# Optimization experiments

Measured on AMD Instinct MI355X. Metric: run time of the kernel, lower is better.

Reference implementation:

```python
import jax, jax.numpy as jnp
import numpy as np

VOXEL_SCALE = 20.0   # cfg.SPARSE3D.VOXEL_SCALE (metric -> voxel pixels)
POOLER_SCALE = 0.25  # cfg.MODEL.ROI_BOX_HEAD.POOLER_SCALES_SPATIAL[0]
RES = 7              # pooler resolution per axis
EPS = 1e-5           # BatchNorm eps


def _roi_align_3d(feat, boxes_px, batch_idx, res):
    """3D ROIAlign, sampling_ratio=1 (one trilinear sample per bin).
    feat: [B, X, Y, Z, C] channels-last; boxes_px: [N,6] = (x1,y1,z1,x2,y2,z2)
    in feature-map coordinates. Returns [N, C, res, res, res]."""
    B, X, Y, Z, C = feat.shape
    N = boxes_px.shape[0]
    start, end = boxes_px[:, :3], boxes_px[:, 3:]
    size = jnp.maximum(end - start, 1.0)            # [N,3] legacy min roi size
    binsz = size / res
    off = jnp.arange(res, dtype=boxes_px.dtype) + 0.5
    px = start[:, 0:1] + off[None, :] * binsz[:, 0:1]   # [N,res]
    py = start[:, 1:2] + off[None, :] * binsz[:, 1:2]
    pz = start[:, 2:3] + off[None, :] * binsz[:, 2:3]
    P = res * res * res
    PX = jnp.broadcast_to(px[:, :, None, None], (N, res, res, res)).reshape(N, P)
    PY = jnp.broadcast_to(py[:, None, :, None], (N, res, res, res)).reshape(N, P)
    PZ = jnp.broadcast_to(pz[:, None, None, :], (N, res, res, res)).reshape(N, P)

    def corners(p, dim):
        p0 = jnp.floor(p)
        frac = p - p0
        i0 = jnp.clip(p0.astype(jnp.int32), 0, dim - 1)
        i1 = jnp.clip(p0.astype(jnp.int32) + 1, 0, dim - 1)
        return i0, i1, frac

    x0, x1, lx = corners(PX, X)
    y0, y1, ly = corners(PY, Y)
    z0, z1, lz = corners(PZ, Z)
    feat_flat = feat.reshape(B * X * Y * Z, C)
    base = batch_idx.astype(jnp.int32)[:, None]          # [N,1]
    acc = jnp.zeros((N, P, C), feat.dtype)
    for dx in (0, 1):  # 8 trilinear corners; fixed small loop
        xi, wx = (x0, 1.0 - lx) if dx == 0 else (x1, lx)
        for dy in (0, 1):
            yi, wy = (y0, 1.0 - ly) if dy == 0 else (y1, ly)
            for dz in (0, 1):
                zi, wz = (z0, 1.0 - lz) if dz == 0 else (z1, lz)
                lin = ((base * X + xi) * Y + yi) * Z + zi  # [N,P]
                acc = acc + (wx * wy * wz)[:, :, None] * feat_flat[lin]
    pooled = acc.reshape(N, res, res, res, C)  # 1 sample per bin -> no avg
    return pooled.transpose(0, 4, 1, 2, 3)     # [N, C, rx, ry, rz]


def setup_inputs():
    key = jax.random.key(0)
    ks = jax.random.split(key, 8)
    B, C, X, Y, Z = 2, 128, 80, 80, 20
    N, rep = 1024, 128 * RES              # rep = OUT_CHANNELS * pooler_z = 896
    in_size = C * RES * RES * RES         # 43904
    features = jax.random.normal(ks[0], (B, X, Y, Z, C), jnp.float32)
    ext = jnp.array([16.0, 16.0, 4.0], jnp.float32)  # metric extent = dim/(voxel_scale*pooler_scale)
    ctr = jax.random.uniform(ks[1], (N, 3), jnp.float32) * ext
    half = 0.25 + jax.random.uniform(ks[2], (N, 3), jnp.float32) * 1.75
    boxes = jnp.concatenate([ctr - half, ctr + half], axis=1)  # metric units
    batch_idx = jax.random.randint(ks[3], (N,), 0, B, jnp.int32)
    conv_w = jax.random.normal(ks[4], (rep, C, RES), jnp.float32) * 0.02
    conv_b = jnp.zeros((rep,), jnp.float32)
    gamma = jnp.ones((rep,), jnp.float32)
    beta = jnp.zeros((rep,), jnp.float32)
    fc6_w = jax.random.normal(ks[5], (in_size, rep), jnp.float32) * np.float32(1.0 / np.sqrt(in_size))
    fc6_b = jnp.zeros((rep,), jnp.float32)
    fc7_w = jax.random.normal(ks[6], (rep, rep), jnp.float32) * np.float32(1.0 / np.sqrt(rep))
    fc7_b = jnp.zeros((rep,), jnp.float32)
    return dict(features=features, boxes=boxes, conv_w=conv_w, conv_b=conv_b,
                gamma=gamma, beta=beta, fc6_w=fc6_w, fc6_b=fc6_b,
                fc7_w=fc7_w, fc7_b=fc7_b, batch_idx=batch_idx)


def reference(features, boxes, conv_w, conv_b, gamma, beta,
              fc6_w, fc6_b, fc7_w, fc7_b, batch_idx):
    # convert_metric_to_pixel (x voxel_scale) fused with pooler spatial scale
    boxes_px = boxes * (VOXEL_SCALE * POOLER_SCALE)
    pooled = _roi_align_3d(features, boxes_px, batch_idx, RES)  # [N,C,7,7,7]
    # conv3d kernel [1,1,Z]: contract channels and z -> [N, rep, 7, 7]
    y = jnp.einsum('ncxyz,rcz->nrxy', pooled, conv_w) + conv_b[None, :, None, None]
    # BatchNorm3d, training-mode batch statistics per channel
    mu = y.mean(axis=(0, 2, 3), keepdims=True)
    var = ((y - mu) ** 2).mean(axis=(0, 2, 3), keepdims=True)
    y = (y - mu) * jax.lax.rsqrt(var + EPS) * gamma[None, :, None, None] + beta[None, :, None, None]
    y = jax.nn.relu(y)
    x2 = y.reshape(y.shape[0], -1)                   # [N, rep*49] == [N, C*343]
    x3 = jax.nn.relu(x2 @ fc6_w + fc6_b)
    x4 = jax.nn.relu(x3 @ fc7_w + fc7_b)
    return x4
```

## Files before the change

### kernel.cpp

```cpp
#include <hip/hip_runtime.h>
#include <cstdint>

typedef unsigned short u16;
using bf16x8  = __attribute__((ext_vector_type(8))) __bf16;
using floatx4 = __attribute__((ext_vector_type(4))) float;

__device__ __forceinline__ u16 f2bf(float f) {
    uint32_t u = __builtin_bit_cast(uint32_t, f);
    u += 0x7fffu + ((u >> 16) & 1u);
    return (u16)(u >> 16);
}
__device__ __forceinline__ float bf2f(u16 h) {
    uint32_t u = ((uint32_t)h) << 16;
    return __builtin_bit_cast(float, u);
}

__device__ __forceinline__ void gl2lds16(const u16* g, u16* l) {
    __builtin_amdgcn_global_load_lds(
        (const __attribute__((address_space(1))) uint32_t*)g,
        (__attribute__((address_space(3))) uint32_t*)l, 16, 0, 0);
}

__global__ __launch_bounds__(256) void k_roialign(
    const float* __restrict__ feat, const float* __restrict__ boxes,
    const int* __restrict__ bidx, u16* __restrict__ A1)
{
    const int n = blockIdx.x;
    const int t = threadIdx.x;
    const float s = 5.0f;
    const float x1 = boxes[n*6+0]*s, y1 = boxes[n*6+1]*s, z1 = boxes[n*6+2]*s;
    const float x2 = boxes[n*6+3]*s, y2 = boxes[n*6+4]*s, z2 = boxes[n*6+5]*s;
    const float binx = fmaxf(x2-x1, 1.0f) * (1.0f/7.0f);
    const float biny = fmaxf(y2-y1, 1.0f) * (1.0f/7.0f);
    const float binz = fmaxf(z2-z1, 1.0f) * (1.0f/7.0f);
    const int b = bidx[n];
    const float* fb = feat + (size_t)b * 80 * 80 * 20 * 128;
    const int c4   = (t & 31) * 4;
    const int slot = t >> 5;

    for (int pair = slot; pair < 49; pair += 8) {
        const int xq = pair / 7;
        const int yq = pair - xq * 7;
        const float px = x1 + ((float)xq + 0.5f) * binx;
        const float py = y1 + ((float)yq + 0.5f) * biny;
        const float fx = floorf(px), fy = floorf(py);
        const float lx = px - fx, ly = py - fy;
        const int xi0 = min(max((int)fx,     0), 79);
        const int xi1 = min(max((int)fx + 1, 0), 79);
        const int yi0 = min(max((int)fy,     0), 79);
        const int yi1 = min(max((int)fy + 1, 0), 79);
        const float wx0 = 1.f-lx, wy0 = 1.f-ly;
        const float w00 = wx0*wy0, w01 = wx0*ly, w10 = lx*wy0, w11 = lx*ly;
        const float* p00 = fb + (size_t)((xi0*80+yi0)*20)*128 + c4;
        const float* p01 = fb + (size_t)((xi0*80+yi1)*20)*128 + c4;
        const float* p10 = fb + (size_t)((xi1*80+yi0)*20)*128 + c4;
        const float* p11 = fb + (size_t)((xi1*80+yi1)*20)*128 + c4;
        u16* orow = A1 + (size_t)(n * 49 + pair) * 896 + c4;
#pragma unroll
        for (int zq = 0; zq < 7; ++zq) {
            const float pz = z1 + ((float)zq + 0.5f) * binz;
            const float fz = floorf(pz);
            const float lz = pz - fz;
            const int zi0 = min(max((int)fz,     0), 19) * 128;
            const int zi1 = min(max((int)fz + 1, 0), 19) * 128;
            const float wz0 = 1.f - lz;
            float a0=0.f, a1=0.f, a2=0.f, a3=0.f;
#define RC(W, P, ZI) { \
            const float4 v = *(const float4*)((P) + (ZI)); \
            a0 = fmaf((W), v.x, a0); a1 = fmaf((W), v.y, a1); \
            a2 = fmaf((W), v.z, a2); a3 = fmaf((W), v.w, a3); }
            RC(w00*wz0, p00, zi0); RC(w00*lz, p00, zi1);
            RC(w01*wz0, p01, zi0); RC(w01*lz, p01, zi1);
            RC(w10*wz0, p10, zi0); RC(w10*lz, p10, zi1);
            RC(w11*wz0, p11, zi0); RC(w11*lz, p11, zi1);
#undef RC
            ushort4 o;
            o.x = f2bf(a0); o.y = f2bf(a1); o.z = f2bf(a2); o.w = f2bf(a3);
            *(ushort4*)(orow + zq * 128) = o;
        }
    }
}

__global__ __launch_bounds__(256) void k_prep_wc(
    const float* __restrict__ w, u16* __restrict__ out)
{
    const int i = blockIdx.x * 256 + threadIdx.x;
    const int r = i / 896, k = i % 896;
    const int z = k >> 7, c = k & 127;
    out[i] = f2bf(w[(r * 128 + c) * 7 + z]);
}

template <int PERM>
__global__ __launch_bounds__(256) void k_transpose(
    const float* __restrict__ in, u16* __restrict__ out, int Kin)
{
    __shared__ u16 tile[64][72];
    const int kp0 = blockIdx.x * 64, r0 = blockIdx.y * 64;
    const int t = threadIdx.x;
#pragma unroll
    for (int it = 0; it < 16; ++it) {
        const int idx = it * 256 + t;
        const int i = idx >> 6, rl = idx & 63;
        const int kp = kp0 + i;
        const int k = PERM ? (kp % 896) * 49 + (kp / 896) : kp;
        tile[i][rl] = f2bf(in[(size_t)k * 896 + r0 + rl]);
    }
    __syncthreads();
#pragma unroll
    for (int it = 0; it < 16; ++it) {
        const int idx = it * 256 + t;
        const int rl = idx >> 6, i = idx & 63;
        out[(size_t)(r0 + rl) * Kin + kp0 + i] = tile[i][rl];
    }
}

template <int EPI>
__global__ __launch_bounds__(256) void k_gemm(
    const u16* __restrict__ A, const u16* __restrict__ Bt,
    float* __restrict__ outF, u16* __restrict__ outH,
    const float* __restrict__ bias, float* __restrict__ bnsum, float* __restrict__ bnsq,
    int Astride, int Bstride, int kpc, int ktot, int partStride)
{
    __shared__ __align__(16) u16 lA[128 * 32];
    __shared__ __align__(16) u16 lB[128 * 32];
    const int t = threadIdx.x;
    const int wave = t >> 6, lane = t & 63;
    const int wm = wave & 1, wn = wave >> 1;
    const int quad = lane >> 4, lr = lane & 15;
    const size_t m0 = (size_t)blockIdx.x * 128;
    const size_t n0 = (size_t)blockIdx.y * 128;
    const int kbeg = blockIdx.z * kpc;
    const int kend = min(kbeg + kpc, ktot);

    floatx4 acc[4][4];
    const floatx4 zero = {0.f, 0.f, 0.f, 0.f};
#pragma unroll
    for (int a = 0; a < 4; ++a)
#pragma unroll
        for (int bq = 0; bq < 4; ++bq) acc[a][bq] = zero;

    const int rs0 = wave * 32 + (lane >> 2);
    const int rs1 = rs0 + 16;
    const int qsw = (lane & 3) ^ ((lane >> 2) & 3);
    const u16* Ab = A + m0 * (size_t)Astride;
    const u16* Bb = Bt + n0 * (size_t)Bstride;
    const u16* srcA0 = Ab + (size_t)rs0 * Astride + qsw * 8;
    const u16* srcA1 = Ab + (size_t)rs1 * Astride + qsw * 8;
    const u16* srcB0 = Bb + (size_t)rs0 * Bstride + qsw * 8;
    const u16* srcB1 = Bb + (size_t)rs1 * Bstride + qsw * 8;
    u16* ldsA0 = lA + (wave * 2 + 0) * 512;
    u16* ldsA1 = lA + (wave * 2 + 1) * 512;
    u16* ldsB0 = lB + (wave * 2 + 0) * 512;
    u16* ldsB1 = lB + (wave * 2 + 1) * 512;

    const int fsw = (quad ^ (lr & 3)) * 8;

    for (int ks = kbeg; ks < kend; ++ks) {
        const size_t k0 = (size_t)ks * 32;
        __syncthreads();
        gl2lds16(srcA0 + k0, ldsA0);
        gl2lds16(srcA1 + k0, ldsA1);
        gl2lds16(srcB0 + k0, ldsB0);
        gl2lds16(srcB1 + k0, ldsB1);
        __syncthreads();
        bf16x8 af[4], bfr[4];
#pragma unroll
        for (int mt = 0; mt < 4; ++mt)
            af[mt] = *(const bf16x8*)(lA + (wm * 64 + mt * 16 + lr) * 32 + fsw);
#pragma unroll
        for (int nt = 0; nt < 4; ++nt)
            bfr[nt] = *(const bf16x8*)(lB + (wn * 64 + nt * 16 + lr) * 32 + fsw);
#pragma unroll
        for (int mt = 0; mt < 4; ++mt)
#pragma unroll
            for (int nt = 0; nt < 4; ++nt)
                acc[mt][nt] = __builtin_amdgcn_mfma_f32_16x16x32_bf16(
                    af[mt], bfr[nt], acc[mt][nt], 0, 0, 0);
    }

    if (EPI == 0) {
#pragma unroll
        for (int nt = 0; nt < 4; ++nt) {
            const int n = (int)n0 + wn * 64 + nt * 16 + lr;
            const float bv = bias[n];
            float s1 = 0.f, s2 = 0.f;
#pragma unroll
            for (int mt = 0; mt < 4; ++mt) {
#pragma unroll
                for (int j = 0; j < 4; ++j) {
                    const int m = (int)m0 + wm * 64 + mt * 16 + quad * 4 + j;
                    const float v = acc[mt][nt][j] + bv;
                    outH[(size_t)m * 896 + n] = f2bf(v);
                    s1 += v;
                    s2 = fmaf(v, v, s2);
                }
            }
            s1 += __shfl_xor(s1, 16); s1 += __shfl_xor(s1, 32);
            s2 += __shfl_xor(s2, 16); s2 += __shfl_xor(s2, 32);
            if (quad == 0) {
                atomicAdd(&bnsum[n], s1);
                atomicAdd(&bnsq[n],  s2);
            }
        }
    } else {
        float* po = outF + (size_t)blockIdx.z * partStride;
#pragma unroll
        for (int nt = 0; nt < 4; ++nt) {
            const int n = (int)n0 + wn * 64 + nt * 16 + lr;
#pragma unroll
            for (int mt = 0; mt < 4; ++mt) {
#pragma unroll
                for (int j = 0; j < 4; ++j) {
                    const int m = (int)m0 + wm * 64 + mt * 16 + quad * 4 + j;
                    po[(size_t)m * 896 + n] = acc[mt][nt][j];
                }
            }
        }
    }
}

__global__ __launch_bounds__(256) void k_bn_apply(
    u16* __restrict__ y, const float* __restrict__ s1, const float* __restrict__ s2,
    const float* __restrict__ gamma, const float* __restrict__ beta)
{
    const size_t i = ((size_t)blockIdx.x * 256 + threadIdx.x) * 8;
    uint4 d = *(const uint4*)(y + i);
    const u16* h = (const u16*)&d;
    const int r0 = (int)(i % 896);
    __align__(16) u16 o[8];
    const float invM = 1.0f / 50176.0f;
#pragma unroll
    for (int j = 0; j < 8; ++j) {
        const int r = r0 + j;
        const float mu  = s1[r] * invM;
        const float var = fmaf(-mu, mu, s2[r] * invM);
        const float rs  = rsqrtf(var + 1e-5f);
        const float v   = (bf2f(h[j]) - mu) * rs * gamma[r] + beta[r];
        o[j] = f2bf(fmaxf(v, 0.f));
    }
    *(uint4*)(y + i) = *(const uint4*)o;
}

__global__ __launch_bounds__(256) void k_x3(
    const float* __restrict__ part, const float* __restrict__ bias, u16* __restrict__ x3)
{
    const size_t i = ((size_t)blockIdx.x * 256 + threadIdx.x) * 4;
    float a0=0.f, a1=0.f, a2=0.f, a3=0.f;
#pragma unroll
    for (int c = 0; c < 16; ++c) {
        const float4 v = *(const float4*)(part + (size_t)c * 917504 + i);
        a0 += v.x; a1 += v.y; a2 += v.z; a3 += v.w;
    }
    const int r = (int)(i % 896);
    ushort4 o;
    o.x = f2bf(fmaxf(a0 + bias[r+0], 0.f));
    o.y = f2bf(fmaxf(a1 + bias[r+1], 0.f));
    o.z = f2bf(fmaxf(a2 + bias[r+2], 0.f));
    o.w = f2bf(fmaxf(a3 + bias[r+3], 0.f));
    *(ushort4*)(x3 + i) = o;
}

__global__ __launch_bounds__(256) void k_out(
    const float* __restrict__ part, const float* __restrict__ bias, float* __restrict__ out)
{
    const size_t i = ((size_t)blockIdx.x * 256 + threadIdx.x) * 4;
    float a0=0.f, a1=0.f, a2=0.f, a3=0.f;
#pragma unroll
    for (int c = 0; c < 4; ++c) {
        const float4 v = *(const float4*)(part + (size_t)c * 917504 + i);
        a0 += v.x; a1 += v.y; a2 += v.z; a3 += v.w;
    }
    const int r = (int)(i % 896);
    float4 o;
    o.x = fmaxf(a0 + bias[r+0], 0.f);
    o.y = fmaxf(a1 + bias[r+1], 0.f);
    o.z = fmaxf(a2 + bias[r+2], 0.f);
    o.w = fmaxf(a3 + bias[r+3], 0.f);
    *(float4*)(out + i) = o;
}

extern "C" void kernel_launch(void* const* d_in, const int* in_sizes, int n_in,
                              void* d_out, int out_size, void* d_ws, size_t ws_size,
                              hipStream_t stream)
{
    (void)in_sizes; (void)n_in; (void)out_size; (void)ws_size;
    const float* features = (const float*)d_in[0];
    const float* boxes    = (const float*)d_in[1];
    const float* conv_w   = (const float*)d_in[2];
    const float* conv_b   = (const float*)d_in[3];
    const float* gamma    = (const float*)d_in[4];
    const float* beta     = (const float*)d_in[5];
    const float* fc6_w    = (const float*)d_in[6];
    const float* fc6_b    = (const float*)d_in[7];
    const float* fc7_w    = (const float*)d_in[8];
    const float* fc7_b    = (const float*)d_in[9];
    const int*   batch_idx = (const int*)d_in[10];
    float* out = (float*)d_out;
    char* ws = (char*)d_ws;

    size_t off = 0;
    auto alloc = [&](size_t b) { size_t o = off; off += (b + 255) & ~(size_t)255; return o; };
    const size_t oA1   = alloc(50176ull * 896 * 2);
    const size_t oWcT  = alloc(896ull * 896 * 2);
    const size_t oY    = alloc(50176ull * 896 * 2);
    const size_t oF6T  = alloc(43904ull * 896 * 2);
    const size_t oF7T  = alloc(896ull * 896 * 2);
    const size_t oStat = alloc(8192);
    const size_t oP2 = oA1;
    const size_t oX3 = oA1 + 58720256;
    const size_t oP3 = oX3 + 1835008;

    u16*   A1    = (u16*)(ws + oA1);
    u16*   WcT   = (u16*)(ws + oWcT);
    u16*   Y     = (u16*)(ws + oY);
    u16*   F6T   = (u16*)(ws + oF6T);
    u16*   F7T   = (u16*)(ws + oF7T);
    float* bnsum = (float*)(ws + oStat);
    float* bnsq  = bnsum + 1024;
    float* P2    = (float*)(ws + oP2);
    u16*   X3    = (u16*)(ws + oX3);
    float* P3    = (float*)(ws + oP3);

    k_prep_wc<<<3136, 256, 0, stream>>>(conv_w, WcT);
    k_transpose<1><<<dim3(686, 14), 256, 0, stream>>>(fc6_w, F6T, 43904);
    k_transpose<0><<<dim3(14, 14), 256, 0, stream>>>(fc7_w, F7T, 896);
    hipMemsetAsync(ws + oStat, 0, 8192, stream);

    k_roialign<<<1024, 256, 0, stream>>>(features, boxes, batch_idx, A1);

    k_gemm<0><<<dim3(392, 7, 1), 256, 0, stream>>>(
        A1, WcT, nullptr, Y, conv_b, bnsum, bnsq, 896, 896, 28, 28, 0);

    k_bn_apply<<<21952, 256, 0, stream>>>(Y, bnsum, bnsq, gamma, beta);

    k_gemm<1><<<dim3(8, 7, 16), 256, 0, stream>>>(
        Y, F6T, P2, nullptr, nullptr, nullptr, nullptr, 43904, 43904, 86, 1372, 917504);
    k_x3<<<896, 256, 0, stream>>>(P2, fc6_b, X3);

    k_gemm<1><<<dim3(8, 7, 4), 256, 0, stream>>>(
        X3, F7T, P3, nullptr, nullptr, nullptr, nullptr, 896, 896, 7, 28, 917504);
    k_out<<<896, 256, 0, stream>>>(P3, fc7_b, out);
}
```

Before: 827.4 us.

## Fuse prep kernels, deepen GEMM K-tile to 64, vectorize epilogue stores

Merges ROIAlign, the conv-weight prep and the fc6/fc7 transposes into one launch that dispatches by block index. The GEMM K-step grows from 32 to 64 with an 8-way XOR swizzle, which halves the barriers per K, and it swaps the MFMA operands so each lane holds 4 consecutive columns. That allows packed uint2 and float4 epilogue stores and per-column shuffle reductions for the BN statistics. The fc6 split-K drops from 16 to 14 partitions, with buffer offsets and the reduce loop adjusted. LDS use per block doubles, which may lower occupancy.

```diff
diff --git a/kernel.cpp b/kernel.cpp
--- a/kernel.cpp
+++ b/kernel.cpp
@@ -21,12 +21,10 @@
         (__attribute__((address_space(3))) uint32_t*)l, 16, 0, 0);
 }
 
-__global__ __launch_bounds__(256) void k_roialign(
-    const float* __restrict__ feat, const float* __restrict__ boxes,
+__device__ void dev_roialign(
+    int n, int t, const float* __restrict__ feat, const float* __restrict__ boxes,
     const int* __restrict__ bidx, u16* __restrict__ A1)
 {
-    const int n = blockIdx.x;
-    const int t = threadIdx.x;
     const float s = 5.0f;
     const float x1 = boxes[n*6+0]*s, y1 = boxes[n*6+1]*s, z1 = boxes[n*6+2]*s;
     const float x2 = boxes[n*6+3]*s, y2 = boxes[n*6+4]*s, z2 = boxes[n*6+5]*s;
@@ -81,22 +79,19 @@
     }
 }
 
-__global__ __launch_bounds__(256) void k_prep_wc(
-    const float* __restrict__ w, u16* __restrict__ out)
-{
-    const int i = blockIdx.x * 256 + threadIdx.x;
+__device__ void dev_prep_wc(int i, const float* __restrict__ w, u16* __restrict__ out)
+{
     const int r = i / 896, k = i % 896;
     const int z = k >> 7, c = k & 127;
     out[i] = f2bf(w[(r * 128 + c) * 7 + z]);
 }
 
 template <int PERM>
-__global__ __launch_bounds__(256) void k_transpose(
-    const float* __restrict__ in, u16* __restrict__ out, int Kin)
-{
-    __shared__ u16 tile[64][72];
-    const int kp0 = blockIdx.x * 64, r0 = blockIdx.y * 64;
-    const int t = threadIdx.x;
+__device__ void dev_transpose(
+    int bx, int by, int t, const float* __restrict__ in, u16* __restrict__ out,
+    int Kin, u16 (*tile)[72])
+{
+    const int kp0 = bx * 64, r0 = by * 64;
 #pragma unroll
     for (int it = 0; it < 16; ++it) {
         const int idx = it * 256 + t;
@@ -114,6 +109,28 @@
     }
 }
 
+__global__ __launch_bounds__(256) void k_prep(
+    const float* __restrict__ feat, const float* __restrict__ boxes,
+    const int* __restrict__ bidx, const float* __restrict__ conv_w,
+    const float* __restrict__ fc6_w, const float* __restrict__ fc7_w,
+    u16* __restrict__ A1, u16* __restrict__ WcT,
+    u16* __restrict__ F6T, u16* __restrict__ F7T)
+{
+    __shared__ u16 tile[64][72];
+    const int b = blockIdx.x, t = threadIdx.x;
+    if (b < 1024) {
+        dev_roialign(b, t, feat, boxes, bidx, A1);
+    } else if (b < 10628) {
+        const int id = b - 1024;
+        dev_transpose<1>(id % 686, id / 686, t, fc6_w, F6T, 43904, tile);
+    } else if (b < 13764) {
+        dev_prep_wc((b - 10628) * 256 + t, conv_w, WcT);
+    } else {
+        const int id = b - 13764;
+        dev_transpose<0>(id % 14, id / 14, t, fc7_w, F7T, 896, tile);
+    }
+}
+
 template <int EPI>
 __global__ __launch_bounds__(256) void k_gemm(
     const u16* __restrict__ A, const u16* __restrict__ Bt,
@@ -121,8 +138,8 @@
     const float* __restrict__ bias, float* __restrict__ bnsum, float* __restrict__ bnsq,
     int Astride, int Bstride, int kpc, int ktot, int partStride)
 {
-    __shared__ __align__(16) u16 lA[128 * 32];
-    __shared__ __align__(16) u16 lB[128 * 32];
+    __shared__ __align__(16) u16 lA[128 * 64];
+    __shared__ __align__(16) u16 lB[128 * 64];
     const int t = threadIdx.x;
     const int wave = t >> 6, lane = t & 63;
     const int wm = wave & 1, wn = wave >> 1;
@@ -139,81 +156,92 @@
 #pragma unroll
         for (int bq = 0; bq < 4; ++bq) acc[a][bq] = zero;
 
-    const int rs0 = wave * 32 + (lane >> 2);
-    const int rs1 = rs0 + 16;
-    const int qsw = (lane & 3) ^ ((lane >> 2) & 3);
+    const int lrow = lane >> 3;
+    const int qsw  = (lane & 7) ^ (lrow & 7);
+    const int rbase = wave * 32 + lrow;
     const u16* Ab = A + m0 * (size_t)Astride;
     const u16* Bb = Bt + n0 * (size_t)Bstride;
-    const u16* srcA0 = Ab + (size_t)rs0 * Astride + qsw * 8;
-    const u16* srcA1 = Ab + (size_t)rs1 * Astride + qsw * 8;
-    const u16* srcB0 = Bb + (size_t)rs0 * Bstride + qsw * 8;
-    const u16* srcB1 = Bb + (size_t)rs1 * Bstride + qsw * 8;
-    u16* ldsA0 = lA + (wave * 2 + 0) * 512;
-    u16* ldsA1 = lA + (wave * 2 + 1) * 512;
-    u16* ldsB0 = lB + (wave * 2 + 0) * 512;
-    u16* ldsB1 = lB + (wave * 2 + 1) * 512;
-
-    const int fsw = (quad ^ (lr & 3)) * 8;
+    const u16* sA = Ab + (size_t)rbase * Astride + qsw * 8;
+    const u16* sB = Bb + (size_t)rbase * Bstride + qsw * 8;
+    u16* dA = lA + wave * 32 * 64;
+    u16* dB = lB + wave * 32 * 64;
+
+    const int rowA = wm * 64 + lr;
+    const int rowB = wn * 64 + lr;
+    const int sw0 = ((quad    ) ^ (lr & 7)) * 8;
+    const int sw1 = ((quad + 4) ^ (lr & 7)) * 8;
 
     for (int ks = kbeg; ks < kend; ++ks) {
-        const size_t k0 = (size_t)ks * 32;
+        const size_t k0 = (size_t)ks * 64;
         __syncthreads();
-        gl2lds16(srcA0 + k0, ldsA0);
-        gl2lds16(srcA1 + k0, ldsA1);
-        gl2lds16(srcB0 + k0, ldsB0);
-        gl2lds16(srcB1 + k0, ldsB1);
+#pragma unroll
+        for (int j2 = 0; j2 < 4; ++j2) {
+            gl2lds16(sA + (size_t)(j2 * 8) * Astride + k0, dA + j2 * 512);
+            gl2lds16(sB + (size_t)(j2 * 8) * Bstride + k0, dB + j2 * 512);
+        }
         __syncthreads();
-        bf16x8 af[4], bfr[4];
-#pragma unroll
-        for (int mt = 0; mt < 4; ++mt)
-            af[mt] = *(const bf16x8*)(lA + (wm * 64 + mt * 16 + lr) * 32 + fsw);
-#pragma unroll
-        for (int nt = 0; nt < 4; ++nt)
-            bfr[nt] = *(const bf16x8*)(lB + (wn * 64 + nt * 16 + lr) * 32 + fsw);
-#pragma unroll
-        for (int mt = 0; mt < 4; ++mt)
+#pragma unroll
+        for (int h = 0; h < 2; ++h) {
+            const int sw = h ? sw1 : sw0;
+            bf16x8 af[4], bfr[4];
+#pragma unroll
+            for (int mt = 0; mt < 4; ++mt)
+                af[mt] = *(const bf16x8*)(lA + (rowA + mt * 16) * 64 + sw);
 #pragma unroll
             for (int nt = 0; nt < 4; ++nt)
-                acc[mt][nt] = __builtin_amdgcn_mfma_f32_16x16x32_bf16(
-                    af[mt], bfr[nt], acc[mt][nt], 0, 0, 0);
+                bfr[nt] = *(const bf16x8*)(lB + (rowB + nt * 16) * 64 + sw);
+#pragma unroll
+            for (int mt = 0; mt < 4; ++mt)
+#pragma unroll
+                for (int nt = 0; nt < 4; ++nt)
+                    acc[mt][nt] = __builtin_amdgcn_mfma_f32_16x16x32_bf16(
+                        bfr[nt], af[mt], acc[mt][nt], 0, 0, 0);
+        }
     }
 
     if (EPI == 0) {
 #pragma unroll
         for (int nt = 0; nt < 4; ++nt) {
-            const int n = (int)n0 + wn * 64 + nt * 16 + lr;
-            const float bv = bias[n];
-            float s1 = 0.f, s2 = 0.f;
+            const int nb = (int)n0 + wn * 64 + nt * 16 + quad * 4;
+            const float4 bv = *(const float4*)(bias + nb);
+            float s1v[4] = {0.f,0.f,0.f,0.f}, s2v[4] = {0.f,0.f,0.f,0.f};
 #pragma unroll
             for (int mt = 0; mt < 4; ++mt) {
-#pragma unroll
-                for (int j = 0; j < 4; ++j) {
-                    const int m = (int)m0 + wm * 64 + mt * 16 + quad * 4 + j;
-                    const float v = acc[mt][nt][j] + bv;
-                    outH[(size_t)m * 896 + n] = f2bf(v);
-                    s1 += v;
-                    s2 = fmaf(v, v, s2);
+                const int m = (int)m0 + wm * 64 + mt * 16 + lr;
+                const float v0 = acc[mt][nt][0] + bv.x;
+                const float v1 = acc[mt][nt][1] + bv.y;
+                const float v2 = acc[mt][nt][2] + bv.z;
+                const float v3 = acc[mt][nt][3] + bv.w;
+                uint2 pk;
+                pk.x = (uint32_t)f2bf(v0) | ((uint32_t)f2bf(v1) << 16);
+                pk.y = (uint32_t)f2bf(v2) | ((uint32_t)f2bf(v3) << 16);
+                *(uint2*)(outH + (size_t)m * 896 + nb) = pk;
+                s1v[0] += v0; s1v[1] += v1; s1v[2] += v2; s1v[3] += v3;
+                s2v[0] = fmaf(v0, v0, s2v[0]); s2v[1] = fmaf(v1, v1, s2v[1]);
+                s2v[2] = fmaf(v2, v2, s2v[2]); s2v[3] = fmaf(v3, v3, s2v[3]);
+            }
+#pragma unroll
+            for (int j = 0; j < 4; ++j) {
+                float a = s1v[j], q = s2v[j];
+                a += __shfl_xor(a, 1); a += __shfl_xor(a, 2);
+                a += __shfl_xor(a, 4); a += __shfl_xor(a, 8);
+                q += __shfl_xor(q, 1); q += __shfl_xor(q, 2);
+                q += __shfl_xor(q, 4); q += __shfl_xor(q, 8);
+                if (lr == 0) {
+                    atomicAdd(&bnsum[nb + j], a);
+                    atomicAdd(&bnsq[nb + j],  q);
                 }
             }
-            s1 += __shfl_xor(s1, 16); s1 += __shfl_xor(s1, 32);
-            s2 += __shfl_xor(s2, 16); s2 += __shfl_xor(s2, 32);
-            if (quad == 0) {
-                atomicAdd(&bnsum[n], s1);
-                atomicAdd(&bnsq[n],  s2);
-            }
         }
     } else {
         float* po = outF + (size_t)blockIdx.z * partStride;
 #pragma unroll
         for (int nt = 0; nt < 4; ++nt) {
-            const int n = (int)n0 + wn * 64 + nt * 16 + lr;
+            const int nb = (int)n0 + wn * 64 + nt * 16 + quad * 4;
 #pragma unroll
             for (int mt = 0; mt < 4; ++mt) {
-#pragma unroll
-                for (int j = 0; j < 4; ++j) {
-                    const int m = (int)m0 + wm * 64 + mt * 16 + quad * 4 + j;
-                    po[(size_t)m * 896 + n] = acc[mt][nt][j];
-                }
+                const int m = (int)m0 + wm * 64 + mt * 16 + lr;
+                *(floatx4*)(po + (size_t)m * 896 + nb) = acc[mt][nt];
             }
         }
     }
@@ -247,7 +275,7 @@
     const size_t i = ((size_t)blockIdx.x * 256 + threadIdx.x) * 4;
     float a0=0.f, a1=0.f, a2=0.f, a3=0.f;
 #pragma unroll
-    for (int c = 0; c < 16; ++c) {
+    for (int c = 0; c < 14; ++c) {
         const float4 v = *(const float4*)(part + (size_t)c * 917504 + i);
         a0 += v.x; a1 += v.y; a2 += v.z; a3 += v.w;
     }
@@ -307,7 +335,7 @@
     const size_t oF7T  = alloc(896ull * 896 * 2);
     const size_t oStat = alloc(8192);
     const size_t oP2 = oA1;
-    const size_t oX3 = oA1 + 58720256;
+    const size_t oX3 = oA1 + 51380224;
     const size_t oP3 = oX3 + 1835008;
 
     u16*   A1    = (u16*)(ws + oA1);
@@ -321,23 +349,21 @@
     u16*   X3    = (u16*)(ws + oX3);
     float* P3    = (float*)(ws + oP3);
 
-    k_prep_wc<<<3136, 256, 0, stream>>>(conv_w, WcT);
-    k_transpose<1><<<dim3(686, 14), 256, 0, stream>>>(fc6_w, F6T, 43904);
-    k_transpose<0><<<dim3(14, 14), 256, 0, stream>>>(fc7_w, F7T, 896);
     hipMemsetAsync(ws + oStat, 0, 8192, stream);
 
-    k_roialign<<<1024, 256, 0, stream>>>(features, boxes, batch_idx, A1);
+    k_prep<<<13960, 256, 0, stream>>>(
+        features, boxes, batch_idx, conv_w, fc6_w, fc7_w, A1, WcT, F6T, F7T);
 
     k_gemm<0><<<dim3(392, 7, 1), 256, 0, stream>>>(
-        A1, WcT, nullptr, Y, conv_b, bnsum, bnsq, 896, 896, 28, 28, 0);
+        A1, WcT, nullptr, Y, conv_b, bnsum, bnsq, 896, 896, 14, 14, 0);
 
     k_bn_apply<<<21952, 256, 0, stream>>>(Y, bnsum, bnsq, gamma, beta);
 
-    k_gemm<1><<<dim3(8, 7, 16), 256, 0, stream>>>(
-        Y, F6T, P2, nullptr, nullptr, nullptr, nullptr, 43904, 43904, 86, 1372, 917504);
+    k_gemm<1><<<dim3(8, 7, 14), 256, 0, stream>>>(
+        Y, F6T, P2, nullptr, nullptr, nullptr, nullptr, 43904, 43904, 49, 686, 917504);
     k_x3<<<896, 256, 0, stream>>>(P2, fc6_b, X3);
 
     k_gemm<1><<<dim3(8, 7, 4), 256, 0, stream>>>(
-        X3, F7T, P3, nullptr, nullptr, nullptr, nullptr, 896, 896, 7, 28, 917504);
+        X3, F7T, P3, nullptr, nullptr, nullptr, nullptr, 896, 896, 4, 14, 917504);
     k_out<<<896, 256, 0, stream>>>(P3, fc7_b, out);
 }
```

New measurement: 1.048 ms. 1.27x slower.
